# Kernel optimization log

Measured on AMD Instinct MI355X. Metric: run time of the kernel, lower is better.

The kernel has to match this reference:

```python
import jax, jax.numpy as jnp
import numpy as np

LATENT_DIM = 8
POLY_DEGREE = 5
DATA_DIM = 64
BATCH = 4096
TOTAL_TERMS = sum(LATENT_DIM ** d for d in range(POLY_DEGREE + 1))  # 37449


def _poly_features(z):
    # z: [B, L] -> [B, sum_d L^d] concatenated Kronecker powers, degree 0..D.
    B = z.shape[0]
    feats = [jnp.ones((B, 1), dtype=z.dtype)]  # degree 0
    cur = z  # degree 1: [B, L]
    feats.append(cur)
    for _ in range(2, POLY_DEGREE + 1):
        # kron(cur, z) per sample: outer product then flatten (row-major matches torch.kron)
        cur = (cur[:, :, None] * z[:, None, :]).reshape(B, -1)
        feats.append(cur)
    return jnp.concatenate(feats, axis=1)  # [B, TOTAL_TERMS]


def setup_inputs() -> dict:
    key = jax.random.key(0)
    k1, k2, k3 = jax.random.split(key, 3)
    z = jax.random.normal(k1, (BATCH, LATENT_DIM), dtype=jnp.float32)
    W = jax.random.normal(k2, (DATA_DIM, TOTAL_TERMS), dtype=jnp.float32) / np.sqrt(TOTAL_TERMS)
    b = jax.random.normal(k3, (DATA_DIM,), dtype=jnp.float32)
    return {"z": z, "W": W, "b": b}


def reference(z, W, b):
    feats = _poly_features(z)                 # [B, TOTAL_TERMS]
    return feats @ W.T + b                    # [B, DATA_DIM]
```

## Files before the change

### kernel.cpp

```cpp
#include <hip/hip_runtime.h>


#define TOTAL_TERMS 37449
#define NBUCKET 1287
#define KPAD 1312
#define FSTRIDE 1320
#define SLOTS_PER_B 120
#define NGRP_OFF 0
#define SLOTS_OFF 4096
#define WT_OFFSET 315392

typedef _Float16 half8 __attribute__((ext_vector_type(8)));
typedef float f32x4 __attribute__((ext_vector_type(4)));

__device__ __constant__ int KSTART[6] = {0, 1, 9, 73, 585, 4681};
__device__ __constant__ int BSTART[6] = {0, 1, 9, 45, 165, 495};
__device__ __constant__ int NTAB[5][8] = {
    {1, 1, 1, 1, 1, 1, 1, 1},
    {8, 7, 6, 5, 4, 3, 2, 1},
    {36, 28, 21, 15, 10, 6, 3, 1},
    {120, 84, 56, 35, 20, 10, 4, 1},
    {330, 210, 126, 70, 35, 15, 5, 1}};
__device__ __constant__ int FACT[6] = {1, 1, 2, 6, 24, 120};

__global__ __launch_bounds__(256) void setup_csr(unsigned short* __restrict__ ngrp,
                                                 unsigned short* __restrict__ slots) {
    int k = blockIdx.x * 256 + threadIdx.x;
    if (k >= TOTAL_TERMS) return;

    int d = 0;
#pragma unroll
    for (int i = 1; i <= 5; ++i)
        if (k >= KSTART[i]) d = i;
    int loc = k - KSTART[d];
    int dgo[5] = {0, 0, 0, 0, 0};
    for (int i = d - 1; i >= 0; --i) { dgo[i] = loc & 7; loc >>= 3; }

    int dg[5];
#pragma unroll
    for (int i = 0; i < 5; ++i) dg[i] = dgo[i];
    for (int i = 1; i < d; ++i) {
        int v = dg[i], j = i;
        while (j > 0 && dg[j - 1] > v) { dg[j] = dg[j - 1]; --j; }
        dg[j] = v;
    }
    int brank = 0, lo = 0;
    for (int i = 0; i < d; ++i) {
        int m = d - 1 - i;
        for (int c = lo; c < dg[i]; ++c) brank += NTAB[m][c];
        lo = dg[i];
    }
    int b = BSTART[d] + brank;

    int mult[8] = {0, 0, 0, 0, 0, 0, 0, 0};
    for (int i = 0; i < d; ++i) mult[dgo[i]]++;
    int D = 1;
#pragma unroll
    for (int c = 0; c < 8; ++c) D *= FACT[mult[c]];
    int cnt = FACT[d] / D;
    int r = 0;
    for (int i = 0; i < d; ++i) {
        int rem = d - 1 - i;
        for (int c = 0; c < dgo[i]; ++c)
            if (mult[c] > 0) r += FACT[rem] * mult[c] / D;
        D /= mult[dgo[i]];
        mult[dgo[i]]--;
    }

    slots[b * SLOTS_PER_B + r] = (unsigned short)k;
    if (r == 0) {
        int ng = (cnt + 7) >> 3;
        ngrp[b] = (unsigned short)ng;
        for (int i = cnt; i < ng * 8; ++i)
            slots[b * SLOTS_PER_B + i] = 0xFFFFu;
    }
}

__global__ __launch_bounds__(256) void fold_gather(const float* __restrict__ W,
                                                   const float* __restrict__ bias,
                                                   const unsigned short* __restrict__ ngrp,
                                                   const unsigned short* __restrict__ slots,
                                                   _Float16* __restrict__ Wt) {
    int lin = blockIdx.x;
    int xcd = lin & 7;
    int g   = lin >> 3;
    int n   = xcd * 8 + g / 6;
    int bx  = g % 6;
    int b   = bx * 256 + threadIdx.x;
    if (b >= KPAD) return;

    float s = 0.f;
    if (b < NBUCKET) {
        const float* Wrow = W + (size_t)n * TOTAL_TERMS;
        const unsigned short* sb = slots + (size_t)b * SLOTS_PER_B;
        int ng = ngrp[b];
        for (int gg = 0; gg < ng; ++gg) {
            uint4 sv = *(const uint4*)(sb + (size_t)gg * 8);
            unsigned k0 = sv.x & 0xFFFFu, k1 = sv.x >> 16;
            unsigned k2 = sv.y & 0xFFFFu, k3 = sv.y >> 16;
            unsigned k4 = sv.z & 0xFFFFu, k5 = sv.z >> 16;
            unsigned k6 = sv.w & 0xFFFFu, k7 = sv.w >> 16;
            float v0 = (k0 != 0xFFFFu) ? Wrow[k0] : 0.f;
            float v1 = (k1 != 0xFFFFu) ? Wrow[k1] : 0.f;
            float v2 = (k2 != 0xFFFFu) ? Wrow[k2] : 0.f;
            float v3 = (k3 != 0xFFFFu) ? Wrow[k3] : 0.f;
            float v4 = (k4 != 0xFFFFu) ? Wrow[k4] : 0.f;
            float v5 = (k5 != 0xFFFFu) ? Wrow[k5] : 0.f;
            float v6 = (k6 != 0xFFFFu) ? Wrow[k6] : 0.f;
            float v7 = (k7 != 0xFFFFu) ? Wrow[k7] : 0.f;
            s += ((v0 + v1) + (v2 + v3)) + ((v4 + v5) + (v6 + v7));
        }
        if (b == 0) s += bias[n];
    }
    int ss = b >> 5, kk = b & 31, quad = kk >> 3, j = kk & 7;
    int lane = (n & 15) + quad * 16;
    Wt[((size_t)((ss * 4 + (n >> 4)) * 64 + lane)) * 8 + j] = (_Float16)s;
}

struct ATab {
    unsigned int t[1344];
    constexpr ATab() : t() {
        int last[1287] = {};
        last[0] = 0;
        for (int c = 0; c < 8; ++c) last[1 + c] = c;
        int starts[6] = {0, 1, 9, 45, 165, 495};
        int pcnt[6] = {0, 0, 64, 128, 352, 800};
        int pos = 0;
        for (int d = 2; d <= 5; ++d) {
            int ps = starts[d - 1], pe = starts[d];
            int dest = starts[d];
            int cnt = 0;
            for (int p = ps; p < pe; ++p)
                for (int c = last[p]; c < 8; ++c) {
                    last[dest] = c;
                    t[pos++] = (unsigned)p | ((unsigned)c << 11) |
                               ((unsigned)dest << 15);
                    ++dest; ++cnt;
                }
            for (; cnt < pcnt[d]; ++cnt)
                t[pos++] = 0u | (0u << 11) | (1311u << 15);
        }
    }
};
__device__ const ATab A_TAB{};

__global__ __launch_bounds__(512) void poly_gemm(const float* __restrict__ z,
                                                 const _Float16* __restrict__ Wt,
                                                 float* __restrict__ out) {
    __shared__ _Float16 feats[16][FSTRIDE];
    __shared__ f32x4 sacc[4][64];
    int tid = threadIdx.x;
    int lane = tid & 63;
    int w = tid >> 6;
    int h = w & 3;
    int kh = w >> 2;
    int mb = blockIdx.x;

    const char* gb = (const char*)Wt + (size_t)(h * 64 + lane) * 16
                   + (size_t)kh * 4096;
    half8 Bk[2][8];
#pragma unroll
    for (int i = 0; i < 8; ++i)
        Bk[0][i] = *(const half8*)(gb + (size_t)i * 8192);

    if (tid < 128) {
        int row = tid >> 3, c = tid & 7;
        float v = z[(size_t)(mb * 16 + row) * 8 + c];
        feats[row][1 + c] = (_Float16)v;
        if (c == 0) feats[row][0] = (_Float16)1.f;
    }

    int sub = tid & 31, row = tid >> 5;
    const int PS[4] = {0, 64, 192, 544};
    const int PTRIP[4] = {2, 4, 11, 25};
#pragma unroll
    for (int dd = 0; dd < 4; ++dd) {
        __syncthreads();
        int base = PS[dd] + sub;
#pragma unroll
        for (int e = 0; e < PTRIP[dd]; ++e) {
            unsigned v = A_TAB.t[base + (e << 5)];
            int p = v & 2047;
            int c = (v >> 11) & 15;
            int dst = v >> 15;
            feats[row][dst] = feats[row][p] * feats[row][1 + c];
        }
    }
    __syncthreads();
    if (sub < 25) feats[row][1287 + sub] = (_Float16)0.f;
    __syncthreads();

    f32x4 acc0 = {0.f, 0.f, 0.f, 0.f}, acc1 = {0.f, 0.f, 0.f, 0.f};
    int q = (lane >> 4) & 3;
    int arow = lane & 15;
    const _Float16* ap = &feats[arow][kh * 32 + q * 8];

#define STEP(i, bank, slot)                                                    \
    {                                                                          \
        half8 av = *(const half8*)(ap + (i) * 64);                             \
        if ((i) & 1)                                                           \
            acc1 = __builtin_amdgcn_mfma_f32_16x16x32_f16(av, Bk[bank][slot],  \
                                                          acc1, 0, 0, 0);      \
        else                                                                   \
            acc0 = __builtin_amdgcn_mfma_f32_16x16x32_f16(av, Bk[bank][slot],  \
                                                          acc0, 0, 0, 0);      \
    }

#pragma unroll
    for (int i = 0; i < 8; ++i)
        Bk[1][i] = *(const half8*)(gb + (size_t)(8 + i) * 8192);
#pragma unroll
    for (int i = 0; i < 8; ++i) STEP(i, 0, i)
#pragma unroll
    for (int i = 0; i < 4; ++i)
        Bk[0][i] = *(const half8*)(gb + (size_t)(16 + i) * 8192);
    if (kh == 0) Bk[0][4] = *(const half8*)(gb + (size_t)20 * 8192);
#pragma unroll
    for (int i = 8; i < 16; ++i) STEP(i, 1, i - 8)
#pragma unroll
    for (int i = 16; i < 20; ++i) STEP(i, 0, i - 16)
    if (kh == 0) STEP(20, 0, 4)
#undef STEP

    f32x4 accf = acc0 + acc1;

    if (kh == 1) sacc[h][lane] = accf;
    __syncthreads();
    if (kh == 0) {
        accf += sacc[h][lane];
        int col = h * 16 + (lane & 15);
        int r0 = mb * 16 + q * 4;
#pragma unroll
        for (int r = 0; r < 4; ++r)
            out[(size_t)(r0 + r) * 64 + col] = accf[r];
    }
}

extern "C" void kernel_launch(void* const* d_in, const int* in_sizes, int n_in,
                              void* d_out, int out_size, void* d_ws, size_t ws_size,
                              hipStream_t stream) {
    (void)in_sizes; (void)n_in; (void)out_size; (void)ws_size;
    const float* z = (const float*)d_in[0];
    const float* W = (const float*)d_in[1];
    const float* b = (const float*)d_in[2];
    float* out = (float*)d_out;

    unsigned short* ngrp  = (unsigned short*)((char*)d_ws + NGRP_OFF);
    unsigned short* slots = (unsigned short*)((char*)d_ws + SLOTS_OFF);
    _Float16* Wt = (_Float16*)((char*)d_ws + WT_OFFSET);

    hipLaunchKernelGGL(setup_csr, dim3((TOTAL_TERMS + 255) / 256), dim3(256), 0,
                       stream, ngrp, slots);
    hipLaunchKernelGGL(fold_gather, dim3(384), dim3(256), 0, stream,
                       W, b, ngrp, slots, Wt);
    hipLaunchKernelGGL(poly_gemm, dim3(256), dim3(512), 0, stream, z, Wt, out);
}
```

Before: 100.2 us.

## Transpose W to fp16 k-major layout before folding, merge CSR setup

```diff
diff --git a/kernel.cpp b/kernel.cpp
--- a/kernel.cpp
+++ b/kernel.cpp
@@ -6,9 +6,12 @@
 #define KPAD 1312
 #define FSTRIDE 1320
 #define SLOTS_PER_B 120
+#define NTB 586
+#define CSRB 147
 #define NGRP_OFF 0
 #define SLOTS_OFF 4096
-#define WT_OFFSET 315392
+#define WT16_OFF 315392
+#define WT_OFFSET 5115904
 
 typedef _Float16 half8 __attribute__((ext_vector_type(8)));
 typedef float f32x4 __attribute__((ext_vector_type(4)));
@@ -23,10 +26,35 @@
     {330, 210, 126, 70, 35, 15, 5, 1}};
 __device__ __constant__ int FACT[6] = {1, 1, 2, 6, 24, 120};
 
-__global__ __launch_bounds__(256) void setup_csr(unsigned short* __restrict__ ngrp,
-                                                 unsigned short* __restrict__ slots) {
-    int k = blockIdx.x * 256 + threadIdx.x;
-    if (k >= TOTAL_TERMS) return;
+__global__ __launch_bounds__(256) void prep(const float* __restrict__ W,
+                                            _Float16* __restrict__ WT16,
+                                            unsigned short* __restrict__ ngrp,
+                                            unsigned short* __restrict__ slots) {
+    int tid = threadIdx.x;
+    if (blockIdx.x < NTB) {
+        __shared__ _Float16 lds[64][66];
+        int lane = tid & 63;
+        int nq   = tid >> 6;
+        int kb   = blockIdx.x * 64;
+        int k    = kb + lane;
+#pragma unroll
+        for (int r = 0; r < 16; ++r) {
+            int n = r * 4 + nq;
+            float v = (k < TOTAL_TERMS) ? W[(size_t)n * TOTAL_TERMS + k] : 0.f;
+            lds[n][lane] = (_Float16)v;
+        }
+        __syncthreads();
+#pragma unroll
+        for (int r = 0; r < 16; ++r) {
+            int kl = r * 4 + nq;
+            WT16[(size_t)(kb + kl) * 64 + lane] = lds[lane][kl];
+        }
+        return;
+    }
+
+    int kk = (blockIdx.x - NTB) * 256 + tid;
+    if (kk >= TOTAL_TERMS) return;
+    int k = kk;
 
     int d = 0;
 #pragma unroll
@@ -76,45 +104,39 @@
     }
 }
 
-__global__ __launch_bounds__(256) void fold_gather(const float* __restrict__ W,
-                                                   const float* __restrict__ bias,
-                                                   const unsigned short* __restrict__ ngrp,
-                                                   const unsigned short* __restrict__ slots,
-                                                   _Float16* __restrict__ Wt) {
-    int lin = blockIdx.x;
-    int xcd = lin & 7;
-    int g   = lin >> 3;
-    int n   = xcd * 8 + g / 6;
-    int bx  = g % 6;
-    int b   = bx * 256 + threadIdx.x;
-    if (b >= KPAD) return;
+__global__ __launch_bounds__(256) void fold(const _Float16* __restrict__ WT16,
+                                            const float* __restrict__ bias,
+                                            const unsigned short* __restrict__ ngrp,
+                                            const unsigned short* __restrict__ slots,
+                                            _Float16* __restrict__ Wt) {
+    int lane = threadIdx.x & 63;
+    int w    = threadIdx.x >> 6;
+    int b    = blockIdx.x * 4 + w;
 
     float s = 0.f;
     if (b < NBUCKET) {
-        const float* Wrow = W + (size_t)n * TOTAL_TERMS;
         const unsigned short* sb = slots + (size_t)b * SLOTS_PER_B;
         int ng = ngrp[b];
         for (int gg = 0; gg < ng; ++gg) {
             uint4 sv = *(const uint4*)(sb + (size_t)gg * 8);
-            unsigned k0 = sv.x & 0xFFFFu, k1 = sv.x >> 16;
-            unsigned k2 = sv.y & 0xFFFFu, k3 = sv.y >> 16;
-            unsigned k4 = sv.z & 0xFFFFu, k5 = sv.z >> 16;
-            unsigned k6 = sv.w & 0xFFFFu, k7 = sv.w >> 16;
-            float v0 = (k0 != 0xFFFFu) ? Wrow[k0] : 0.f;
-            float v1 = (k1 != 0xFFFFu) ? Wrow[k1] : 0.f;
-            float v2 = (k2 != 0xFFFFu) ? Wrow[k2] : 0.f;
-            float v3 = (k3 != 0xFFFFu) ? Wrow[k3] : 0.f;
-            float v4 = (k4 != 0xFFFFu) ? Wrow[k4] : 0.f;
-            float v5 = (k5 != 0xFFFFu) ? Wrow[k5] : 0.f;
-            float v6 = (k6 != 0xFFFFu) ? Wrow[k6] : 0.f;
-            float v7 = (k7 != 0xFFFFu) ? Wrow[k7] : 0.f;
-            s += ((v0 + v1) + (v2 + v3)) + ((v4 + v5) + (v6 + v7));
-        }
-        if (b == 0) s += bias[n];
+            unsigned ks[8];
+            ks[0] = sv.x & 0xFFFFu; ks[1] = sv.x >> 16;
+            ks[2] = sv.y & 0xFFFFu; ks[3] = sv.y >> 16;
+            ks[4] = sv.z & 0xFFFFu; ks[5] = sv.z >> 16;
+            ks[6] = sv.w & 0xFFFFu; ks[7] = sv.w >> 16;
+            float v[8];
+#pragma unroll
+            for (int j = 0; j < 8; ++j)
+                v[j] = (ks[j] != 0xFFFFu)
+                         ? (float)WT16[(size_t)ks[j] * 64 + lane] : 0.f;
+            s += ((v[0] + v[1]) + (v[2] + v[3])) +
+                 ((v[4] + v[5]) + (v[6] + v[7]));
+        }
+        if (b == 0) s += bias[lane];
     }
     int ss = b >> 5, kk = b & 31, quad = kk >> 3, j = kk & 7;
-    int lane = (n & 15) + quad * 16;
-    Wt[((size_t)((ss * 4 + (n >> 4)) * 64 + lane)) * 8 + j] = (_Float16)s;
+    int fl = (lane & 15) + quad * 16;
+    Wt[((size_t)((ss * 4 + (lane >> 4)) * 64 + fl)) * 8 + j] = (_Float16)s;
 }
 
 struct ATab {
@@ -247,11 +269,12 @@
 
     unsigned short* ngrp  = (unsigned short*)((char*)d_ws + NGRP_OFF);
     unsigned short* slots = (unsigned short*)((char*)d_ws + SLOTS_OFF);
-    _Float16* Wt = (_Float16*)((char*)d_ws + WT_OFFSET);
-
-    hipLaunchKernelGGL(setup_csr, dim3((TOTAL_TERMS + 255) / 256), dim3(256), 0,
-                       stream, ngrp, slots);
-    hipLaunchKernelGGL(fold_gather, dim3(384), dim3(256), 0, stream,
-                       W, b, ngrp, slots, Wt);
+    _Float16* WT16 = (_Float16*)((char*)d_ws + WT16_OFF);
+    _Float16* Wt   = (_Float16*)((char*)d_ws + WT_OFFSET);
+
+    hipLaunchKernelGGL(prep, dim3(NTB + CSRB), dim3(256), 0, stream,
+                       W, WT16, ngrp, slots);
+    hipLaunchKernelGGL(fold, dim3(KPAD / 4), dim3(256), 0, stream,
+                       WT16, b, ngrp, slots, Wt);
     hipLaunchKernelGGL(poly_gemm, dim3(256), dim3(512), 0, stream, z, Wt, out);
 }
```

Measured after the change: 122.1 us. 1.22x slower.
